# Kernel optimization log

Measured on AMD Instinct MI355X. Metric: run time of the kernel, lower is better.

The kernel has to match this reference:

```python
import jax, jax.numpy as jnp
import numpy as np

# dims / hyperparams (mirror init_kwargs)
B, N, C, K = 256, 16000, 32, 64          # batch, samples, cochlear channels, gammatone taps
FS, FMIN, FMAX, BWF = 16000, 100.0, 8000.0, 1.0
WINDOW, STRIDE = 256, 128                # inner hair cell framing -> T = 124
ANS, HID, OUT = 10, 50, 10               # auditory-nerve fanout, bushy/ic hidden, AC out
BETA, THR = 0.95, 1.0                    # snn.Leaky(beta=0.95), threshold 1.0, subtract reset
AN_LO, AN_HI, AN_THR = 0.5, 1.5, 0.5     # an_range scales + AN firing threshold

# Heaviside spike with ATan surrogate gradient (snntorch default style)
@jax.custom_vjp
def spike(u):
    return (u > 0).astype(u.dtype)

def _spike_fwd(u):
    return spike(u), u

def _spike_bwd(u, g):
    return (g / (1.0 + (jnp.pi * u) ** 2),)

spike.defvjp(_spike_fwd, _spike_bwd)

def _gammatone_bank():
    # ERB-spaced 4th-order gammatone impulse responses, unit L2 norm. [C, K]
    def hz2erb(f):
        return 21.4 * np.log10(1.0 + 0.00437 * f)
    def erb2hz(e):
        return (10.0 ** (e / 21.4) - 1.0) / 0.00437
    cfs = erb2hz(np.linspace(hz2erb(FMIN), hz2erb(FMAX), C))
    b = BWF * 1.019 * 24.7 * (4.37 * cfs / 1000.0 + 1.0)
    t = np.arange(K) / FS
    ker = (t[None, :] ** 3) * np.exp(-2 * np.pi * b[:, None] * t[None, :]) \
          * np.cos(2 * np.pi * cfs[:, None] * t[None, :])
    ker = ker / (np.linalg.norm(ker, axis=1, keepdims=True) + 1e-12)
    return jnp.asarray(ker, jnp.float32)

def setup_inputs() -> dict:
    key = jax.random.key(0)
    k1, k2, k3, k4 = jax.random.split(key, 4)
    audio = jax.random.normal(k1, (B, N), dtype=jnp.float32)
    W_bushy = jax.random.normal(k2, (HID, C * ANS), dtype=jnp.float32) / np.sqrt(C * ANS)
    W_ic = jax.random.normal(k3, (HID, HID), dtype=jnp.float32) / np.sqrt(HID)
    W_ac = jax.random.normal(k4, (OUT, HID), dtype=jnp.float32) / np.sqrt(HID)
    return {"audio": audio, "gt_kernels": _gammatone_bank(),
            "W_bushy": W_bushy, "W_ic": W_ic, "W_ac": W_ac}

def reference(audio, gt_kernels, W_bushy, W_ic, W_ac):
    # Cochlear: gammatone filterbank, [B,1,N] conv [C,1,K] SAME -> [B,C,N]
    y = jax.lax.conv_general_dilated(audio[:, None, :], gt_kernels[:, None, :],
                                     window_strides=(1,), padding="SAME")
    # InnerHairCell: half-wave rectify + moving-average framing -> [B,C,T]
    y = jnp.maximum(y, 0.0)
    env = jax.lax.reduce_window(y, 0.0, jax.lax.add,
                                (1, 1, WINDOW), (1, 1, STRIDE), "VALID") / WINDOW
    frames = jnp.transpose(env, (2, 0, 1))  # [T,B,C]
    scales = jnp.linspace(AN_LO, AN_HI, ANS, dtype=jnp.float32)

    def lif(mem, cur):
        mem = BETA * mem + cur
        spk = spike(mem - THR)
        return spk, mem - THR * spk  # subtract reset

    def step(carry, x_t):  # x_t [B,C]
        mem_b, mem_ic, mem_ac = carry
        # AuditoryNerve: ans scaled copies per channel, threshold fire -> [B, C*ANS]
        spk_an = spike(x_t[:, :, None] * scales - AN_THR).reshape(x_t.shape[0], -1)
        spk_b, mem_b = lif(mem_b, spk_an @ W_bushy.T)     # Bushy
        spk_ic, mem_ic = lif(mem_ic, spk_b @ W_ic.T)      # InferiorColliculus
        spk_ac, mem_ac = lif(mem_ac, spk_ic @ W_ac.T)     # AudioCortex
        return (mem_b, mem_ic, mem_ac), (spk_ac, mem_ac)

    bsz = audio.shape[0]
    init = (jnp.zeros((bsz, HID), audio.dtype),
            jnp.zeros((bsz, HID), audio.dtype),
            jnp.zeros((bsz, OUT), audio.dtype))
    _, (spk_rec, mem_rec) = jax.lax.scan(step, init, frames)
    # stack along dim=1 as in torch code -> [B,T,OUT]
    return jnp.transpose(spk_rec, (1, 0, 2)), jnp.transpose(mem_rec, (1, 0, 2))
```

## Files before the change

### kernel.cpp

```cpp
#include <hip/hip_runtime.h>

#define B_   256
#define N_   16000
#define C_   32
#define K_   64
#define T_   124
#define NJ   125
#define HID_ 50
#define OUT_ 10
#define TB_  1024
#define CURS 52
#define WBS  324

typedef unsigned int u32;
typedef float v2f __attribute__((ext_vector_type(2)));
struct __align__(16) f2x2 { v2f lo, hi; };

__device__ __forceinline__ float fadd(float a, float b) { return __fadd_rn(a, b); }
__device__ __forceinline__ float fmul(float a, float b) { return __fmul_rn(a, b); }
__device__ __forceinline__ float fsub(float a, float b) { return __fsub_rn(a, b); }

__device__ __forceinline__ void PKFMA(v2f& y, v2f a, const f2x2& T, int k) {
    switch (k) {
    case 0:  asm("v_pk_fma_f32 %0, %1, %2, %0 op_sel:[0,0,0] op_sel_hi:[1,0,1]"
                 : "+v"(y) : "v"(a), "s"(T.lo)); break;
    case 1:  asm("v_pk_fma_f32 %0, %1, %2, %0 op_sel:[0,1,0] op_sel_hi:[1,1,1]"
                 : "+v"(y) : "v"(a), "s"(T.lo)); break;
    case 2:  asm("v_pk_fma_f32 %0, %1, %2, %0 op_sel:[0,0,0] op_sel_hi:[1,0,1]"
                 : "+v"(y) : "v"(a), "s"(T.hi)); break;
    default: asm("v_pk_fma_f32 %0, %1, %2, %0 op_sel:[0,1,0] op_sel_hi:[1,1,1]"
                 : "+v"(y) : "v"(a), "s"(T.hi)); break;
    }
}

__global__ __launch_bounds__(256, 4) void convA(const float* __restrict__ audio,
                                                const float* __restrict__ gt,
                                                float* __restrict__ Sg) {
    __shared__ __align__(16) float abI[1280];
    __shared__ __align__(16) float ybuf[4][4][272];

    const int b = blockIdx.x, g = blockIdx.y;
    const int tid = threadIdx.x, w = tid >> 6, lane = tid & 63;
    const float* arow = audio + (size_t)b * N_;

    const int origin = (g << 10) - 32;
    for (int idx = tid; idx < 1280; idx += 256) {
        int P = idx / 640, j = idx - P * 640;
        int ii = j >> 1, h = j & 1;
        int gi = origin + (P << 9) + (h << 8) + ii;
        float v = (gi >= 0 && gi < N_) ? arow[gi] : 0.0f;
        abI[P * 640 + (j ^ (((j >> 5) & 1) << 2))] = v;
    }
    __syncthreads();

    for (int G = 0; G < 2; ++G) {
        const int rowbase = __builtin_amdgcn_readfirstlane(((w << 3) + (G << 2)) << 6);
        const float* kg = gt + rowbase;

        v2f Y[2][4][4];
#pragma unroll
        for (int P = 0; P < 2; ++P)
#pragma unroll
            for (int ch = 0; ch < 4; ++ch)
#pragma unroll
                for (int d = 0; d < 4; ++d) { Y[P][ch][d].x = 0.0f; Y[P][ch][d].y = 0.0f; }

        {
            f2x2 Tc[4];
#pragma unroll
            for (int ch = 0; ch < 4; ++ch)
                Tc[ch] = *(const f2x2*)(kg + (ch << 6));
            const int u = lane;
            const int p1 = (u << 3) ^ (((u >> 2) & 1) << 2);
#pragma unroll
            for (int P = 0; P < 2; ++P) {
                const float* abP = abI + P * 640;
                const f2x2 A0 = *(const f2x2*)(abP + p1);
                const f2x2 A1 = *(const f2x2*)(abP + (p1 ^ 4));
#pragma unroll
                for (int e = 0; e < 4; ++e) {
                    const v2f a = (e == 0) ? A0.lo : (e == 1) ? A0.hi
                                : (e == 2) ? A1.lo : A1.hi;
#pragma unroll
                    for (int ch = 0; ch < 4; ++ch)
#pragma unroll
                        for (int d = 0; d < 4; ++d) {
                            const int kb = e - 1 - d;
                            if (kb >= 0) PKFMA(Y[P][ch][d], a, Tc[ch], kb);
                        }
                }
            }
        }

#pragma unroll 1
        for (int q = 1; q < 16; ++q) {
            f2x2 Tm[4], Tc[4];
#pragma unroll
            for (int ch = 0; ch < 4; ++ch) {
                Tm[ch] = *(const f2x2*)(kg + (ch << 6) + ((q - 1) << 2));
                Tc[ch] = *(const f2x2*)(kg + (ch << 6) + (q << 2));
            }
            const int u = lane + q;
            const int p1 = (u << 3) ^ (((u >> 2) & 1) << 2);
#pragma unroll
            for (int P = 0; P < 2; ++P) {
                const float* abP = abI + P * 640;
                const f2x2 A0 = *(const f2x2*)(abP + p1);
                const f2x2 A1 = *(const f2x2*)(abP + (p1 ^ 4));
#pragma unroll
                for (int e = 0; e < 4; ++e) {
                    const v2f a = (e == 0) ? A0.lo : (e == 1) ? A0.hi
                                : (e == 2) ? A1.lo : A1.hi;
#pragma unroll
                    for (int ch = 0; ch < 4; ++ch)
#pragma unroll
                        for (int d = 0; d < 4; ++d) {
                            const int ts = e - 1 - d;
                            if (ts >= 0) PKFMA(Y[P][ch][d], a, Tc[ch], ts);
                            else         PKFMA(Y[P][ch][d], a, Tm[ch], 4 + ts);
                        }
                }
            }
        }

        {
            f2x2 Tm[4];
#pragma unroll
            for (int ch = 0; ch < 4; ++ch)
                Tm[ch] = *(const f2x2*)(kg + (ch << 6) + 60);
            const int u = lane + 16;
            const int p1 = (u << 3) ^ (((u >> 2) & 1) << 2);
#pragma unroll
            for (int P = 0; P < 2; ++P) {
                const float* abP = abI + P * 640;
                const f2x2 A0 = *(const f2x2*)(abP + p1);
                const f2x2 A1 = *(const f2x2*)(abP + (p1 ^ 4));
#pragma unroll
                for (int e = 0; e < 4; ++e) {
                    const v2f a = (e == 0) ? A0.lo : (e == 1) ? A0.hi
                                : (e == 2) ? A1.lo : A1.hi;
#pragma unroll
                    for (int ch = 0; ch < 4; ++ch)
#pragma unroll
                        for (int d = 0; d < 4; ++d) {
                            const int ts = e - 1 - d;
                            if (ts < 0) PKFMA(Y[P][ch][d], a, Tm[ch], 4 + ts);
                        }
                }
            }
        }

#pragma unroll
        for (int pp = 0; pp < 4; ++pp) {
            const int P = pp >> 1, h = pp & 1;
#pragma unroll
            for (int ch = 0; ch < 4; ++ch) {
                float4 z;
                z.x = fmaxf(h ? Y[P][ch][0].y : Y[P][ch][0].x, 0.0f);
                z.y = fmaxf(h ? Y[P][ch][1].y : Y[P][ch][1].x, 0.0f);
                z.z = fmaxf(h ? Y[P][ch][2].y : Y[P][ch][2].x, 0.0f);
                z.w = fmaxf(h ? Y[P][ch][3].y : Y[P][ch][3].x, 0.0f);
                *(float4*)(&ybuf[w][ch][((lane >> 5) * 136) + ((lane & 31) << 2)]) = z;
            }
            {
                const int ch2 = lane >> 4, blk = (lane >> 3) & 1, j = lane & 7;
                const float* yb = &ybuf[w][ch2][blk * 136 + j];
                float r = yb[0];
#pragma unroll
                for (int m = 1; m < 16; ++m) r = fadd(r, yb[m << 3]);
                float v = fadd(r, __shfl_xor(r, 1));
                v = fadd(v, __shfl_xor(v, 2));
                v = fadd(v, __shfl_xor(v, 4));
                const int jg = (g << 3) + (pp << 1) + blk;
                const int c = (w << 3) + (G << 2) + ch2;
                if (j == 0 && jg < NJ) Sg[((size_t)b * C_ + c) * NJ + jg] = v;
            }
        }
    }
}

__global__ __launch_bounds__(TB_, 1) void snnB(const float* __restrict__ Sg,
                                               const float* __restrict__ Wb,
                                               const float* __restrict__ Wic,
                                               const float* __restrict__ Wac,
                                               float* __restrict__ out) {
    __shared__ __align__(16) float sWb[HID_ * WBS];
    __shared__ __align__(16) float sWic[HID_ * 52];
    __shared__ __align__(16) float sWac[OUT_ * 52];
    __shared__ u32   mask[128 * 10];
    __shared__ __align__(16) float cur[T_ * CURS];
    __shared__ __align__(16) float icur[T_ * CURS];
    __shared__ float acur[T_ * 12];

    const int b = blockIdx.x, tid = threadIdx.x;

    for (int i4 = tid; i4 < 4000; i4 += TB_) {
        const int i = i4 << 2;
        const int r = i / 320, col = i - r * 320;
        *(float4*)(&sWb[r * WBS + col]) = *(const float4*)(Wb + i);
    }
    for (int i = tid; i < HID_ * HID_; i += TB_) {
        int r = i / 50;
        sWic[r * 52 + (i - r * 50)] = Wic[i];
    }
    for (int i = tid; i < OUT_ * HID_; i += TB_) {
        int r = i / 50;
        sWac[r * 52 + (i - r * 50)] = Wac[i];
    }

    const float* Sb = Sg + (size_t)b * C_ * NJ;
    for (int idx = tid; idx < 1280; idx += TB_) {
        if (idx >= T_ * 10) { mask[idx] = 0; continue; }
        int t = idx / 10, wd = idx - t * 10;
        u32 m = 0;
        int c_prev = -1;
        float env = 0.0f;
        for (int k = 0; k < 32; ++k) {
            int i = wd * 32 + k;
            int c = i / 10, s = i - c * 10;
            if (c != c_prev) {
                env = fmul(fadd(Sb[c * NJ + t], Sb[c * NJ + t + 1]), 0.00390625f);
                c_prev = c;
            }
            float sf = (s == 9) ? 1.5f : (float)(0.5 + (double)s * (1.0 / 9.0));
            if (fsub(fmul(env, sf), 0.5f) > 0.0f) m |= (1u << k);
        }
        mask[idx] = m;
    }
    __syncthreads();

    if (tid < 31 * 25) {
        const int t0 = tid / 25, hp = tid - t0 * 25;
        const float* wr0 = sWb + hp * WBS;
        const float* wr1 = sWb + (hp + 25) * WBS;
        const u32* mrow = mask + t0 * 10;
        v2f a0 = {0.0f, 0.0f}, a1 = {0.0f, 0.0f};
        v2f a2 = {0.0f, 0.0f}, a3 = {0.0f, 0.0f};
#pragma unroll 1
        for (int wi = 0; wi < 10; ++wi) {
            const u32 w0 = mrow[wi],       w1 = mrow[310 + wi];
            const u32 w2 = mrow[620 + wi], w3 = mrow[930 + wi];
#pragma unroll
            for (int b2 = 0; b2 < 32; ++b2) {
                const int i = (wi << 5) + b2;
                const int iw0 = __float_as_int(wr0[i]);
                const int iw1 = __float_as_int(wr1[i]);
                const int s0 = __builtin_amdgcn_sbfe((int)w0, b2, 1);
                const int s1 = __builtin_amdgcn_sbfe((int)w1, b2, 1);
                const int s2 = __builtin_amdgcn_sbfe((int)w2, b2, 1);
                const int s3 = __builtin_amdgcn_sbfe((int)w3, b2, 1);
                v2f p0, p1, p2, p3;
                p0.x = __int_as_float(iw0 & s0);  p0.y = __int_as_float(iw1 & s0);
                p1.x = __int_as_float(iw0 & s1);  p1.y = __int_as_float(iw1 & s1);
                p2.x = __int_as_float(iw0 & s2);  p2.y = __int_as_float(iw1 & s2);
                p3.x = __int_as_float(iw0 & s3);  p3.y = __int_as_float(iw1 & s3);
                a0 = a0 + p0;
                a1 = a1 + p1;
                a2 = a2 + p2;
                a3 = a3 + p3;
            }
        }
        cur[(t0     ) * CURS + hp] = a0.x;  cur[(t0     ) * CURS + hp + 25] = a0.y;
        cur[(t0 + 31) * CURS + hp] = a1.x;  cur[(t0 + 31) * CURS + hp + 25] = a1.y;
        cur[(t0 + 62) * CURS + hp] = a2.x;  cur[(t0 + 62) * CURS + hp + 25] = a2.y;
        cur[(t0 + 93) * CURS + hp] = a3.x;  cur[(t0 + 93) * CURS + hp + 25] = a3.y;
    }
    __syncthreads();

    if (tid < HID_) {
        float mem = 0.0f;
        for (int t0 = 0; t0 < 120; t0 += 8) {
            float c0[8];
#pragma unroll
            for (int k = 0; k < 8; ++k) c0[k] = cur[(t0 + k) * CURS + tid];
#pragma unroll
            for (int k = 0; k < 8; ++k) {
                float m = fadd(fmul(0.95f, mem), c0[k]);
                float sp = (fsub(m, 1.0f) > 0.0f) ? 1.0f : 0.0f;
                mem = fsub(m, sp);
                cur[(t0 + k) * CURS + tid] = sp;
            }
        }
        for (int t = 120; t < T_; ++t) {
            float m = fadd(fmul(0.95f, mem), cur[t * CURS + tid]);
            float sp = (fsub(m, 1.0f) > 0.0f) ? 1.0f : 0.0f;
            mem = fsub(m, sp);
            cur[t * CURS + tid] = sp;
        }
    }
    __syncthreads();

    if (tid < 31 * 25) {
        const int t0 = tid / 25, hp = tid - t0 * 25;
        const float* w0 = sWic + hp * 52;
        const float* w1 = sWic + (hp + 25) * 52;
        const float* sb0 = cur + (t0     ) * CURS;
        const float* sb1 = cur + (t0 + 31) * CURS;
        const float* sb2 = cur + (t0 + 62) * CURS;
        const float* sb3 = cur + (t0 + 93) * CURS;
        float A00 = 0.0f, A01 = 0.0f, A10 = 0.0f, A11 = 0.0f;
        float A20 = 0.0f, A21 = 0.0f, A30 = 0.0f, A31 = 0.0f;
#pragma unroll
        for (int g4 = 0; g4 < 12; ++g4) {
            const float4 wa = *(const float4*)(w0 + (g4 << 2));
            const float4 wb = *(const float4*)(w1 + (g4 << 2));
            const float4 s0 = *(const float4*)(sb0 + (g4 << 2));
            const float4 s1 = *(const float4*)(sb1 + (g4 << 2));
            const float4 s2 = *(const float4*)(sb2 + (g4 << 2));
            const float4 s3 = *(const float4*)(sb3 + (g4 << 2));
            A00 = fmaf(s0.x, wa.x, A00); A00 = fmaf(s0.y, wa.y, A00);
            A00 = fmaf(s0.z, wa.z, A00); A00 = fmaf(s0.w, wa.w, A00);
            A01 = fmaf(s0.x, wb.x, A01); A01 = fmaf(s0.y, wb.y, A01);
            A01 = fmaf(s0.z, wb.z, A01); A01 = fmaf(s0.w, wb.w, A01);
            A10 = fmaf(s1.x, wa.x, A10); A10 = fmaf(s1.y, wa.y, A10);
            A10 = fmaf(s1.z, wa.z, A10); A10 = fmaf(s1.w, wa.w, A10);
            A11 = fmaf(s1.x, wb.x, A11); A11 = fmaf(s1.y, wb.y, A11);
            A11 = fmaf(s1.z, wb.z, A11); A11 = fmaf(s1.w, wb.w, A11);
            A20 = fmaf(s2.x, wa.x, A20); A20 = fmaf(s2.y, wa.y, A20);
            A20 = fmaf(s2.z, wa.z, A20); A20 = fmaf(s2.w, wa.w, A20);
            A21 = fmaf(s2.x, wb.x, A21); A21 = fmaf(s2.y, wb.y, A21);
            A21 = fmaf(s2.z, wb.z, A21); A21 = fmaf(s2.w, wb.w, A21);
            A30 = fmaf(s3.x, wa.x, A30); A30 = fmaf(s3.y, wa.y, A30);
            A30 = fmaf(s3.z, wa.z, A30); A30 = fmaf(s3.w, wa.w, A30);
            A31 = fmaf(s3.x, wb.x, A31); A31 = fmaf(s3.y, wb.y, A31);
            A31 = fmaf(s3.z, wb.z, A31); A31 = fmaf(s3.w, wb.w, A31);
        }
        A00 = fmaf(sb0[48], w0[48], A00); A00 = fmaf(sb0[49], w0[49], A00);
        A01 = fmaf(sb0[48], w1[48], A01); A01 = fmaf(sb0[49], w1[49], A01);
        A10 = fmaf(sb1[48], w0[48], A10); A10 = fmaf(sb1[49], w0[49], A10);
        A11 = fmaf(sb1[48], w1[48], A11); A11 = fmaf(sb1[49], w1[49], A11);
        A20 = fmaf(sb2[48], w0[48], A20); A20 = fmaf(sb2[49], w0[49], A20);
        A21 = fmaf(sb2[48], w1[48], A21); A21 = fmaf(sb2[49], w1[49], A21);
        A30 = fmaf(sb3[48], w0[48], A30); A30 = fmaf(sb3[49], w0[49], A30);
        A31 = fmaf(sb3[48], w1[48], A31); A31 = fmaf(sb3[49], w1[49], A31);
        icur[(t0     ) * CURS + hp] = A00;  icur[(t0     ) * CURS + hp + 25] = A01;
        icur[(t0 + 31) * CURS + hp] = A10;  icur[(t0 + 31) * CURS + hp + 25] = A11;
        icur[(t0 + 62) * CURS + hp] = A20;  icur[(t0 + 62) * CURS + hp + 25] = A21;
        icur[(t0 + 93) * CURS + hp] = A30;  icur[(t0 + 93) * CURS + hp + 25] = A31;
    }
    __syncthreads();

    if (tid < HID_) {
        float mem = 0.0f;
        for (int t0 = 0; t0 < 120; t0 += 8) {
            float c0[8];
#pragma unroll
            for (int k = 0; k < 8; ++k) c0[k] = icur[(t0 + k) * CURS + tid];
#pragma unroll
            for (int k = 0; k < 8; ++k) {
                float m = fadd(fmul(0.95f, mem), c0[k]);
                float sp = (fsub(m, 1.0f) > 0.0f) ? 1.0f : 0.0f;
                mem = fsub(m, sp);
                icur[(t0 + k) * CURS + tid] = sp;
            }
        }
        for (int t = 120; t < T_; ++t) {
            float m = fadd(fmul(0.95f, mem), icur[t * CURS + tid]);
            float sp = (fsub(m, 1.0f) > 0.0f) ? 1.0f : 0.0f;
            mem = fsub(m, sp);
            icur[t * CURS + tid] = sp;
        }
    }
    __syncthreads();

    if (tid < 31 * 5) {
        const int t0 = tid / 5, op = tid - t0 * 5;
        const float* w0 = sWac + op * 52;
        const float* w1 = sWac + (op + 5) * 52;
        const float* sb0 = icur + (t0     ) * CURS;
        const float* sb1 = icur + (t0 + 31) * CURS;
        const float* sb2 = icur + (t0 + 62) * CURS;
        const float* sb3 = icur + (t0 + 93) * CURS;
        float A00 = 0.0f, A01 = 0.0f, A10 = 0.0f, A11 = 0.0f;
        float A20 = 0.0f, A21 = 0.0f, A30 = 0.0f, A31 = 0.0f;
#pragma unroll
        for (int g4 = 0; g4 < 12; ++g4) {
            const float4 wa = *(const float4*)(w0 + (g4 << 2));
            const float4 wb = *(const float4*)(w1 + (g4 << 2));
            const float4 s0 = *(const float4*)(sb0 + (g4 << 2));
            const float4 s1 = *(const float4*)(sb1 + (g4 << 2));
            const float4 s2 = *(const float4*)(sb2 + (g4 << 2));
            const float4 s3 = *(const float4*)(sb3 + (g4 << 2));
            A00 = fmaf(s0.x, wa.x, A00); A00 = fmaf(s0.y, wa.y, A00);
            A00 = fmaf(s0.z, wa.z, A00); A00 = fmaf(s0.w, wa.w, A00);
            A01 = fmaf(s0.x, wb.x, A01); A01 = fmaf(s0.y, wb.y, A01);
            A01 = fmaf(s0.z, wb.z, A01); A01 = fmaf(s0.w, wb.w, A01);
            A10 = fmaf(s1.x, wa.x, A10); A10 = fmaf(s1.y, wa.y, A10);
            A10 = fmaf(s1.z, wa.z, A10); A10 = fmaf(s1.w, wa.w, A10);
            A11 = fmaf(s1.x, wb.x, A11); A11 = fmaf(s1.y, wb.y, A11);
            A11 = fmaf(s1.z, wb.z, A11); A11 = fmaf(s1.w, wb.w, A11);
            A20 = fmaf(s2.x, wa.x, A20); A20 = fmaf(s2.y, wa.y, A20);
            A20 = fmaf(s2.z, wa.z, A20); A20 = fmaf(s2.w, wa.w, A20);
            A21 = fmaf(s2.x, wb.x, A21); A21 = fmaf(s2.y, wb.y, A21);
            A21 = fmaf(s2.z, wb.z, A21); A21 = fmaf(s2.w, wb.w, A21);
            A30 = fmaf(s3.x, wa.x, A30); A30 = fmaf(s3.y, wa.y, A30);
            A30 = fmaf(s3.z, wa.z, A30); A30 = fmaf(s3.w, wa.w, A30);
            A31 = fmaf(s3.x, wb.x, A31); A31 = fmaf(s3.y, wb.y, A31);
            A31 = fmaf(s3.z, wb.z, A31); A31 = fmaf(s3.w, wb.w, A31);
        }
        A00 = fmaf(sb0[48], w0[48], A00); A00 = fmaf(sb0[49], w0[49], A00);
        A01 = fmaf(sb0[48], w1[48], A01); A01 = fmaf(sb0[49], w1[49], A01);
        A10 = fmaf(sb1[48], w0[48], A10); A10 = fmaf(sb1[49], w0[49], A10);
        A11 = fmaf(sb1[48], w1[48], A11); A11 = fmaf(sb1[49], w1[49], A11);
        A20 = fmaf(sb2[48], w0[48], A20); A20 = fmaf(sb2[49], w0[49], A20);
        A21 = fmaf(sb2[48], w1[48], A21); A21 = fmaf(sb2[49], w1[49], A21);
        A30 = fmaf(sb3[48], w0[48], A30); A30 = fmaf(sb3[49], w0[49], A30);
        A31 = fmaf(sb3[48], w1[48], A31); A31 = fmaf(sb3[49], w1[49], A31);
        acur[(t0     ) * 12 + op] = A00;  acur[(t0     ) * 12 + op + 5] = A01;
        acur[(t0 + 31) * 12 + op] = A10;  acur[(t0 + 31) * 12 + op + 5] = A11;
        acur[(t0 + 62) * 12 + op] = A20;  acur[(t0 + 62) * 12 + op + 5] = A21;
        acur[(t0 + 93) * 12 + op] = A30;  acur[(t0 + 93) * 12 + op + 5] = A31;
    }
    __syncthreads();

    if (tid < OUT_) {
        float mem = 0.0f;
        for (int t0 = 0; t0 < 120; t0 += 8) {
            float c0[8];
#pragma unroll
            for (int k = 0; k < 8; ++k) c0[k] = acur[(t0 + k) * 12 + tid];
#pragma unroll
            for (int k = 0; k < 8; ++k) {
                float m = fadd(fmul(0.95f, mem), c0[k]);
                float sp = (fsub(m, 1.0f) > 0.0f) ? 1.0f : 0.0f;
                float mo = fsub(m, sp);
                mem = mo;
                size_t base = ((size_t)b * T_ + (t0 + k)) * OUT_ + tid;
                out[base] = sp;
                out[(size_t)(B_ * T_ * OUT_) + base] = mo;
            }
        }
        for (int t = 120; t < T_; ++t) {
            float m = fadd(fmul(0.95f, mem), acur[t * 12 + tid]);
            float sp = (fsub(m, 1.0f) > 0.0f) ? 1.0f : 0.0f;
            float mo = fsub(m, sp);
            mem = mo;
            size_t base = ((size_t)b * T_ + t) * OUT_ + tid;
            out[base] = sp;
            out[(size_t)(B_ * T_ * OUT_) + base] = mo;
        }
    }
}

extern "C" void kernel_launch(void* const* d_in, const int* in_sizes, int n_in,
                              void* d_out, int out_size, void* d_ws, size_t ws_size,
                              hipStream_t stream) {
    (void)in_sizes; (void)n_in; (void)out_size; (void)ws_size;
    const float* audio = (const float*)d_in[0];
    const float* gt    = (const float*)d_in[1];
    const float* Wb    = (const float*)d_in[2];
    const float* Wic   = (const float*)d_in[3];
    const float* Wac   = (const float*)d_in[4];

    float* Sg = (float*)d_ws;

    convA<<<dim3(B_, 16), dim3(256), 0, stream>>>(audio, gt, Sg);
    snnB<<<dim3(B_), dim3(TB_), 0, stream>>>(Sg, Wb, Wic, Wac, (float*)d_out);
}
```

Before: 290.7 us.

## Split SNN kernel into time-parallel bushy-current kernel and recurrent kernel

The single per-batch SNN kernel is split in two. The first kernel computes the bushy-layer input currents with two blocks per batch item, each covering half of the timesteps, and writes them to workspace memory. The second kernel loads those currents and runs the recurrent LIF layers. This spreads the dominant masked matmul over twice as many blocks to use more CUs, at the cost of an extra launch and a global round-trip for the currents. The original fused kernel is kept as a fallback when the workspace is too small.

Result: no change. 285.9 us (-1.7%).

```diff
diff --git a/kernel.cpp b/kernel.cpp
--- a/kernel.cpp
+++ b/kernel.cpp
@@ -11,6 +11,7 @@
 #define TB_  1024
 #define CURS 52
 #define WBS  324
+#define TSPAN 62
 
 typedef unsigned int u32;
 typedef float v2f __attribute__((ext_vector_type(2)));
@@ -179,39 +180,27 @@
     }
 }
 
-__global__ __launch_bounds__(TB_, 1) void snnB(const float* __restrict__ Sg,
-                                               const float* __restrict__ Wb,
-                                               const float* __restrict__ Wic,
-                                               const float* __restrict__ Wac,
-                                               float* __restrict__ out) {
+__global__ __launch_bounds__(1024, 8) void snnB1(const float* __restrict__ Sg,
+                                                 const float* __restrict__ Wb,
+                                                 float* __restrict__ cur2) {
     __shared__ __align__(16) float sWb[HID_ * WBS];
-    __shared__ __align__(16) float sWic[HID_ * 52];
-    __shared__ __align__(16) float sWac[OUT_ * 52];
-    __shared__ u32   mask[128 * 10];
-    __shared__ __align__(16) float cur[T_ * CURS];
-    __shared__ __align__(16) float icur[T_ * CURS];
-    __shared__ float acur[T_ * 12];
-
-    const int b = blockIdx.x, tid = threadIdx.x;
-
-    for (int i4 = tid; i4 < 4000; i4 += TB_) {
+    __shared__ u32 mask[64 * 10];
+
+    const int b = blockIdx.x, tg = blockIdx.y;
+    const int tid = threadIdx.x;
+    const int tbase = tg * TSPAN;
+
+    for (int i4 = tid; i4 < 4000; i4 += 1024) {
         const int i = i4 << 2;
         const int r = i / 320, col = i - r * 320;
         *(float4*)(&sWb[r * WBS + col]) = *(const float4*)(Wb + i);
     }
-    for (int i = tid; i < HID_ * HID_; i += TB_) {
-        int r = i / 50;
-        sWic[r * 52 + (i - r * 50)] = Wic[i];
-    }
-    for (int i = tid; i < OUT_ * HID_; i += TB_) {
-        int r = i / 50;
-        sWac[r * 52 + (i - r * 50)] = Wac[i];
-    }
 
     const float* Sb = Sg + (size_t)b * C_ * NJ;
-    for (int idx = tid; idx < 1280; idx += TB_) {
-        if (idx >= T_ * 10) { mask[idx] = 0; continue; }
-        int t = idx / 10, wd = idx - t * 10;
+    for (int idx = tid; idx < 640; idx += 1024) {
+        if (idx >= TSPAN * 10) { mask[idx] = 0; continue; }
+        int tl = idx / 10, wd = idx - tl * 10;
+        int t = tbase + tl;
         u32 m = 0;
         int c_prev = -1;
         float env = 0.0f;
@@ -230,40 +219,59 @@
     __syncthreads();
 
     if (tid < 31 * 25) {
-        const int t0 = tid / 25, hp = tid - t0 * 25;
+        const int tl = tid / 25, hp = tid - tl * 25;
         const float* wr0 = sWb + hp * WBS;
         const float* wr1 = sWb + (hp + 25) * WBS;
-        const u32* mrow = mask + t0 * 10;
-        v2f a0 = {0.0f, 0.0f}, a1 = {0.0f, 0.0f};
-        v2f a2 = {0.0f, 0.0f}, a3 = {0.0f, 0.0f};
+        const u32* mA = mask + tl * 10;
+        const u32* mB = mask + (tl + 31) * 10;
+        v2f A0 = {0.0f, 0.0f}, A1 = {0.0f, 0.0f};
 #pragma unroll 1
         for (int wi = 0; wi < 10; ++wi) {
-            const u32 w0 = mrow[wi],       w1 = mrow[310 + wi];
-            const u32 w2 = mrow[620 + wi], w3 = mrow[930 + wi];
+            const u32 wa = mA[wi], wc = mB[wi];
 #pragma unroll
             for (int b2 = 0; b2 < 32; ++b2) {
                 const int i = (wi << 5) + b2;
                 const int iw0 = __float_as_int(wr0[i]);
                 const int iw1 = __float_as_int(wr1[i]);
-                const int s0 = __builtin_amdgcn_sbfe((int)w0, b2, 1);
-                const int s1 = __builtin_amdgcn_sbfe((int)w1, b2, 1);
-                const int s2 = __builtin_amdgcn_sbfe((int)w2, b2, 1);
-                const int s3 = __builtin_amdgcn_sbfe((int)w3, b2, 1);
-                v2f p0, p1, p2, p3;
-                p0.x = __int_as_float(iw0 & s0);  p0.y = __int_as_float(iw1 & s0);
-                p1.x = __int_as_float(iw0 & s1);  p1.y = __int_as_float(iw1 & s1);
-                p2.x = __int_as_float(iw0 & s2);  p2.y = __int_as_float(iw1 & s2);
-                p3.x = __int_as_float(iw0 & s3);  p3.y = __int_as_float(iw1 & s3);
-                a0 = a0 + p0;
-                a1 = a1 + p1;
-                a2 = a2 + p2;
-                a3 = a3 + p3;
-            }
-        }
-        cur[(t0     ) * CURS + hp] = a0.x;  cur[(t0     ) * CURS + hp + 25] = a0.y;
-        cur[(t0 + 31) * CURS + hp] = a1.x;  cur[(t0 + 31) * CURS + hp + 25] = a1.y;
-        cur[(t0 + 62) * CURS + hp] = a2.x;  cur[(t0 + 62) * CURS + hp + 25] = a2.y;
-        cur[(t0 + 93) * CURS + hp] = a3.x;  cur[(t0 + 93) * CURS + hp + 25] = a3.y;
+                const int sa = __builtin_amdgcn_sbfe((int)wa, b2, 1);
+                const int sc = __builtin_amdgcn_sbfe((int)wc, b2, 1);
+                v2f p0, p1;
+                p0.x = __int_as_float(iw0 & sa);  p0.y = __int_as_float(iw1 & sa);
+                p1.x = __int_as_float(iw0 & sc);  p1.y = __int_as_float(iw1 & sc);
+                A0 = A0 + p0;
+                A1 = A1 + p1;
+            }
+        }
+        float* cb = cur2 + ((size_t)b * T_ + tbase) * HID_;
+        cb[(tl     ) * HID_ + hp] = A0.x;  cb[(tl     ) * HID_ + hp + 25] = A0.y;
+        cb[(tl + 31) * HID_ + hp] = A1.x;  cb[(tl + 31) * HID_ + hp + 25] = A1.y;
+    }
+}
+
+__global__ __launch_bounds__(1024, 1) void snnB2(const float* __restrict__ cur2,
+                                                 const float* __restrict__ Wic,
+                                                 const float* __restrict__ Wac,
+                                                 float* __restrict__ out) {
+    __shared__ __align__(16) float sWic[HID_ * 52];
+    __shared__ __align__(16) float sWac[OUT_ * 52];
+    __shared__ __align__(16) float cur[T_ * CURS];
+    __shared__ __align__(16) float icur[T_ * CURS];
+    __shared__ float acur[T_ * 12];
+
+    const int b = blockIdx.x, tid = threadIdx.x;
+
+    for (int i = tid; i < HID_ * HID_; i += 1024) {
+        int r = i / 50;
+        sWic[r * 52 + (i - r * 50)] = Wic[i];
+    }
+    for (int i = tid; i < OUT_ * HID_; i += 1024) {
+        int r = i / 50;
+        sWac[r * 52 + (i - r * 50)] = Wac[i];
+    }
+    const float* cb = cur2 + (size_t)b * T_ * HID_;
+    for (int j = tid; j < T_ * 25; j += 1024) {
+        int t = j / 25, h2 = (j - t * 25) << 1;
+        *(float2*)(&cur[t * CURS + h2]) = *(const float2*)(cb + t * HID_ + h2);
     }
     __syncthreads();
 
@@ -442,10 +450,273 @@
     }
 }
 
+__global__ __launch_bounds__(TB_, 1) void snnB(const float* __restrict__ Sg,
+                                               const float* __restrict__ Wb,
+                                               const float* __restrict__ Wic,
+                                               const float* __restrict__ Wac,
+                                               float* __restrict__ out) {
+    __shared__ __align__(16) float sWb[HID_ * WBS];
+    __shared__ __align__(16) float sWic[HID_ * 52];
+    __shared__ __align__(16) float sWac[OUT_ * 52];
+    __shared__ u32   mask[128 * 10];
+    __shared__ __align__(16) float cur[T_ * CURS];
+    __shared__ __align__(16) float icur[T_ * CURS];
+    __shared__ float acur[T_ * 12];
+
+    const int b = blockIdx.x, tid = threadIdx.x;
+
+    for (int i4 = tid; i4 < 4000; i4 += TB_) {
+        const int i = i4 << 2;
+        const int r = i / 320, col = i - r * 320;
+        *(float4*)(&sWb[r * WBS + col]) = *(const float4*)(Wb + i);
+    }
+    for (int i = tid; i < HID_ * HID_; i += TB_) {
+        int r = i / 50;
+        sWic[r * 52 + (i - r * 50)] = Wic[i];
+    }
+    for (int i = tid; i < OUT_ * HID_; i += TB_) {
+        int r = i / 50;
+        sWac[r * 52 + (i - r * 50)] = Wac[i];
+    }
+
+    const float* Sb = Sg + (size_t)b * C_ * NJ;
+    for (int idx = tid; idx < 1280; idx += TB_) {
+        if (idx >= T_ * 10) { mask[idx] = 0; continue; }
+        int t = idx / 10, wd = idx - t * 10;
+        u32 m = 0;
+        int c_prev = -1;
+        float env = 0.0f;
+        for (int k = 0; k < 32; ++k) {
+            int i = wd * 32 + k;
+            int c = i / 10, s = i - c * 10;
+            if (c != c_prev) {
+                env = fmul(fadd(Sb[c * NJ + t], Sb[c * NJ + t + 1]), 0.00390625f);
+                c_prev = c;
+            }
+            float sf = (s == 9) ? 1.5f : (float)(0.5 + (double)s * (1.0 / 9.0));
+            if (fsub(fmul(env, sf), 0.5f) > 0.0f) m |= (1u << k);
+        }
+        mask[idx] = m;
+    }
+    __syncthreads();
+
+    if (tid < 31 * 25) {
+        const int t0 = tid / 25, hp = tid - t0 * 25;
+        const float* wr0 = sWb + hp * WBS;
+        const float* wr1 = sWb + (hp + 25) * WBS;
+        const u32* mrow = mask + t0 * 10;
+        v2f a0 = {0.0f, 0.0f}, a1 = {0.0f, 0.0f};
+        v2f a2 = {0.0f, 0.0f}, a3 = {0.0f, 0.0f};
+#pragma unroll 1
+        for (int wi = 0; wi < 10; ++wi) {
+            const u32 w0 = mrow[wi],       w1 = mrow[310 + wi];
+            const u32 w2 = mrow[620 + wi], w3 = mrow[930 + wi];
+#pragma unroll
+            for (int b2 = 0; b2 < 32; ++b2) {
+                const int i = (wi << 5) + b2;
+                const int iw0 = __float_as_int(wr0[i]);
+                const int iw1 = __float_as_int(wr1[i]);
+                const int s0 = __builtin_amdgcn_sbfe((int)w0, b2, 1);
+                const int s1 = __builtin_amdgcn_sbfe((int)w1, b2, 1);
+                const int s2 = __builtin_amdgcn_sbfe((int)w2, b2, 1);
+                const int s3 = __builtin_amdgcn_sbfe((int)w3, b2, 1);
+                v2f p0, p1, p2, p3;
+                p0.x = __int_as_float(iw0 & s0);  p0.y = __int_as_float(iw1 & s0);
+                p1.x = __int_as_float(iw0 & s1);  p1.y = __int_as_float(iw1 & s1);
+                p2.x = __int_as_float(iw0 & s2);  p2.y = __int_as_float(iw1 & s2);
+                p3.x = __int_as_float(iw0 & s3);  p3.y = __int_as_float(iw1 & s3);
+                a0 = a0 + p0;
+                a1 = a1 + p1;
+                a2 = a2 + p2;
+                a3 = a3 + p3;
+            }
+        }
+        cur[(t0     ) * CURS + hp] = a0.x;  cur[(t0     ) * CURS + hp + 25] = a0.y;
+        cur[(t0 + 31) * CURS + hp] = a1.x;  cur[(t0 + 31) * CURS + hp + 25] = a1.y;
+        cur[(t0 + 62) * CURS + hp] = a2.x;  cur[(t0 + 62) * CURS + hp + 25] = a2.y;
+        cur[(t0 + 93) * CURS + hp] = a3.x;  cur[(t0 + 93) * CURS + hp + 25] = a3.y;
+    }
+    __syncthreads();
+
+    if (tid < HID_) {
+        float mem = 0.0f;
+        for (int t0 = 0; t0 < 120; t0 += 8) {
+            float c0[8];
+#pragma unroll
+            for (int k = 0; k < 8; ++k) c0[k] = cur[(t0 + k) * CURS + tid];
+#pragma unroll
+            for (int k = 0; k < 8; ++k) {
+                float m = fadd(fmul(0.95f, mem), c0[k]);
+                float sp = (fsub(m, 1.0f) > 0.0f) ? 1.0f : 0.0f;
+                mem = fsub(m, sp);
+                cur[(t0 + k) * CURS + tid] = sp;
+            }
+        }
+        for (int t = 120; t < T_; ++t) {
+            float m = fadd(fmul(0.95f, mem), cur[t * CURS + tid]);
+            float sp = (fsub(m, 1.0f) > 0.0f) ? 1.0f : 0.0f;
+            mem = fsub(m, sp);
+            cur[t * CURS + tid] = sp;
+        }
+    }
+    __syncthreads();
+
+    if (tid < 31 * 25) {
+        const int t0 = tid / 25, hp = tid - t0 * 25;
+        const float* w0 = sWic + hp * 52;
+        const float* w1 = sWic + (hp + 25) * 52;
+        const float* sb0 = cur + (t0     ) * CURS;
+        const float* sb1 = cur + (t0 + 31) * CURS;
+        const float* sb2 = cur + (t0 + 62) * CURS;
+        const float* sb3 = cur + (t0 + 93) * CURS;
+        float A00 = 0.0f, A01 = 0.0f, A10 = 0.0f, A11 = 0.0f;
+        float A20 = 0.0f, A21 = 0.0f, A30 = 0.0f, A31 = 0.0f;
+#pragma unroll
+        for (int g4 = 0; g4 < 12; ++g4) {
+            const float4 wa = *(const float4*)(w0 + (g4 << 2));
+            const float4 wb = *(const float4*)(w1 + (g4 << 2));
+            const float4 s0 = *(const float4*)(sb0 + (g4 << 2));
+            const float4 s1 = *(const float4*)(sb1 + (g4 << 2));
+            const float4 s2 = *(const float4*)(sb2 + (g4 << 2));
+            const float4 s3 = *(const float4*)(sb3 + (g4 << 2));
+            A00 = fmaf(s0.x, wa.x, A00); A00 = fmaf(s0.y, wa.y, A00);
+            A00 = fmaf(s0.z, wa.z, A00); A00 = fmaf(s0.w, wa.w, A00);
+            A01 = fmaf(s0.x, wb.x, A01); A01 = fmaf(s0.y, wb.y, A01);
+            A01 = fmaf(s0.z, wb.z, A01); A01 = fmaf(s0.w, wb.w, A01);
+            A10 = fmaf(s1.x, wa.x, A10); A10 = fmaf(s1.y, wa.y, A10);
+            A10 = fmaf(s1.z, wa.z, A10); A10 = fmaf(s1.w, wa.w, A10);
+            A11 = fmaf(s1.x, wb.x, A11); A11 = fmaf(s1.y, wb.y, A11);
+            A11 = fmaf(s1.z, wb.z, A11); A11 = fmaf(s1.w, wb.w, A11);
+            A20 = fmaf(s2.x, wa.x, A20); A20 = fmaf(s2.y, wa.y, A20);
+            A20 = fmaf(s2.z, wa.z, A20); A20 = fmaf(s2.w, wa.w, A20);
+            A21 = fmaf(s2.x, wb.x, A21); A21 = fmaf(s2.y, wb.y, A21);
+            A21 = fmaf(s2.z, wb.z, A21); A21 = fmaf(s2.w, wb.w, A21);
+            A30 = fmaf(s3.x, wa.x, A30); A30 = fmaf(s3.y, wa.y, A30);
+            A30 = fmaf(s3.z, wa.z, A30); A30 = fmaf(s3.w, wa.w, A30);
+            A31 = fmaf(s3.x, wb.x, A31); A31 = fmaf(s3.y, wb.y, A31);
+            A31 = fmaf(s3.z, wb.z, A31); A31 = fmaf(s3.w, wb.w, A31);
+        }
+        A00 = fmaf(sb0[48], w0[48], A00); A00 = fmaf(sb0[49], w0[49], A00);
+        A01 = fmaf(sb0[48], w1[48], A01); A01 = fmaf(sb0[49], w1[49], A01);
+        A10 = fmaf(sb1[48], w0[48], A10); A10 = fmaf(sb1[49], w0[49], A10);
+        A11 = fmaf(sb1[48], w1[48], A11); A11 = fmaf(sb1[49], w1[49], A11);
+        A20 = fmaf(sb2[48], w0[48], A20); A20 = fmaf(sb2[49], w0[49], A20);
+        A21 = fmaf(sb2[48], w1[48], A21); A21 = fmaf(sb2[49], w1[49], A21);
+        A30 = fmaf(sb3[48], w0[48], A30); A30 = fmaf(sb3[49], w0[49], A30);
+        A31 = fmaf(sb3[48], w1[48], A31); A31 = fmaf(sb3[49], w1[49], A31);
+        icur[(t0     ) * CURS + hp] = A00;  icur[(t0     ) * CURS + hp + 25] = A01;
+        icur[(t0 + 31) * CURS + hp] = A10;  icur[(t0 + 31) * CURS + hp + 25] = A11;
+        icur[(t0 + 62) * CURS + hp] = A20;  icur[(t0 + 62) * CURS + hp + 25] = A21;
+        icur[(t0 + 93) * CURS + hp] = A30;  icur[(t0 + 93) * CURS + hp + 25] = A31;
+    }
+    __syncthreads();
+
+    if (tid < HID_) {
+        float mem = 0.0f;
+        for (int t0 = 0; t0 < 120; t0 += 8) {
+            float c0[8];
+#pragma unroll
+            for (int k = 0; k < 8; ++k) c0[k] = icur[(t0 + k) * CURS + tid];
+#pragma unroll
+            for (int k = 0; k < 8; ++k) {
+                float m = fadd(fmul(0.95f, mem), c0[k]);
+                float sp = (fsub(m, 1.0f) > 0.0f) ? 1.0f : 0.0f;
+                mem = fsub(m, sp);
+                icur[(t0 + k) * CURS + tid] = sp;
+            }
+        }
+        for (int t = 120; t < T_; ++t) {
+            float m = fadd(fmul(0.95f, mem), icur[t * CURS + tid]);
+            float sp = (fsub(m, 1.0f) > 0.0f) ? 1.0f : 0.0f;
+            mem = fsub(m, sp);
+            icur[t * CURS + tid] = sp;
+        }
+    }
+    __syncthreads();
+
+    if (tid < 31 * 5) {
+        const int t0 = tid / 5, op = tid - t0 * 5;
+        const float* w0 = sWac + op * 52;
+        const float* w1 = sWac + (op + 5) * 52;
+        const float* sb0 = icur + (t0     ) * CURS;
+        const float* sb1 = icur + (t0 + 31) * CURS;
+        const float* sb2 = icur + (t0 + 62) * CURS;
+        const float* sb3 = icur + (t0 + 93) * CURS;
+        float A00 = 0.0f, A01 = 0.0f, A10 = 0.0f, A11 = 0.0f;
+        float A20 = 0.0f, A21 = 0.0f, A30 = 0.0f, A31 = 0.0f;
+#pragma unroll
+        for (int g4 = 0; g4 < 12; ++g4) {
+            const float4 wa = *(const float4*)(w0 + (g4 << 2));
+            const float4 wb = *(const float4*)(w1 + (g4 << 2));
+            const float4 s0 = *(const float4*)(sb0 + (g4 << 2));
+            const float4 s1 = *(const float4*)(sb1 + (g4 << 2));
+            const float4 s2 = *(const float4*)(sb2 + (g4 << 2));
+            const float4 s3 = *(const float4*)(sb3 + (g4 << 2));
+            A00 = fmaf(s0.x, wa.x, A00); A00 = fmaf(s0.y, wa.y, A00);
+            A00 = fmaf(s0.z, wa.z, A00); A00 = fmaf(s0.w, wa.w, A00);
+            A01 = fmaf(s0.x, wb.x, A01); A01 = fmaf(s0.y, wb.y, A01);
+            A01 = fmaf(s0.z, wb.z, A01); A01 = fmaf(s0.w, wb.w, A01);
+            A10 = fmaf(s1.x, wa.x, A10); A10 = fmaf(s1.y, wa.y, A10);
+            A10 = fmaf(s1.z, wa.z, A10); A10 = fmaf(s1.w, wa.w, A10);
+            A11 = fmaf(s1.x, wb.x, A11); A11 = fmaf(s1.y, wb.y, A11);
+            A11 = fmaf(s1.z, wb.z, A11); A11 = fmaf(s1.w, wb.w, A11);
+            A20 = fmaf(s2.x, wa.x, A20); A20 = fmaf(s2.y, wa.y, A20);
+            A20 = fmaf(s2.z, wa.z, A20); A20 = fmaf(s2.w, wa.w, A20);
+            A21 = fmaf(s2.x, wb.x, A21); A21 = fmaf(s2.y, wb.y, A21);
+            A21 = fmaf(s2.z, wb.z, A21); A21 = fmaf(s2.w, wb.w, A21);
+            A30 = fmaf(s3.x, wa.x, A30); A30 = fmaf(s3.y, wa.y, A30);
+            A30 = fmaf(s3.z, wa.z, A30); A30 = fmaf(s3.w, wa.w, A30);
+            A31 = fmaf(s3.x, wb.x, A31); A31 = fmaf(s3.y, wb.y, A31);
+            A31 = fmaf(s3.z, wb.z, A31); A31 = fmaf(s3.w, wb.w, A31);
+        }
+        A00 = fmaf(sb0[48], w0[48], A00); A00 = fmaf(sb0[49], w0[49], A00);
+        A01 = fmaf(sb0[48], w1[48], A01); A01 = fmaf(sb0[49], w1[49], A01);
+        A10 = fmaf(sb1[48], w0[48], A10); A10 = fmaf(sb1[49], w0[49], A10);
+        A11 = fmaf(sb1[48], w1[48], A11); A11 = fmaf(sb1[49], w1[49], A11);
+        A20 = fmaf(sb2[48], w0[48], A20); A20 = fmaf(sb2[49], w0[49], A20);
+        A21 = fmaf(sb2[48], w1[48], A21); A21 = fmaf(sb2[49], w1[49], A21);
+        A30 = fmaf(sb3[48], w0[48], A30); A30 = fmaf(sb3[49], w0[49], A30);
+        A31 = fmaf(sb3[48], w1[48], A31); A31 = fmaf(sb3[49], w1[49], A31);
+        acur[(t0     ) * 12 + op] = A00;  acur[(t0     ) * 12 + op + 5] = A01;
+        acur[(t0 + 31) * 12 + op] = A10;  acur[(t0 + 31) * 12 + op + 5] = A11;
+        acur[(t0 + 62) * 12 + op] = A20;  acur[(t0 + 62) * 12 + op + 5] = A21;
+        acur[(t0 + 93) * 12 + op] = A30;  acur[(t0 + 93) * 12 + op + 5] = A31;
+    }
+    __syncthreads();
+
+    if (tid < OUT_) {
+        float mem = 0.0f;
+        for (int t0 = 0; t0 < 120; t0 += 8) {
+            float c0[8];
+#pragma unroll
+            for (int k = 0; k < 8; ++k) c0[k] = acur[(t0 + k) * 12 + tid];
+#pragma unroll
+            for (int k = 0; k < 8; ++k) {
+                float m = fadd(fmul(0.95f, mem), c0[k]);
+                float sp = (fsub(m, 1.0f) > 0.0f) ? 1.0f : 0.0f;
+                float mo = fsub(m, sp);
+                mem = mo;
+                size_t base = ((size_t)b * T_ + (t0 + k)) * OUT_ + tid;
+                out[base] = sp;
+                out[(size_t)(B_ * T_ * OUT_) + base] = mo;
+            }
+        }
+        for (int t = 120; t < T_; ++t) {
+            float m = fadd(fmul(0.95f, mem), acur[t * 12 + tid]);
+            float sp = (fsub(m, 1.0f) > 0.0f) ? 1.0f : 0.0f;
+            float mo = fsub(m, sp);
+            mem = mo;
+            size_t base = ((size_t)b * T_ + t) * OUT_ + tid;
+            out[base] = sp;
+            out[(size_t)(B_ * T_ * OUT_) + base] = mo;
+        }
+    }
+}
+
 extern "C" void kernel_launch(void* const* d_in, const int* in_sizes, int n_in,
                               void* d_out, int out_size, void* d_ws, size_t ws_size,
                               hipStream_t stream) {
-    (void)in_sizes; (void)n_in; (void)out_size; (void)ws_size;
+    (void)in_sizes; (void)n_in; (void)out_size;
     const float* audio = (const float*)d_in[0];
     const float* gt    = (const float*)d_in[1];
     const float* Wb    = (const float*)d_in[2];
@@ -453,7 +724,16 @@
     const float* Wac   = (const float*)d_in[4];
 
     float* Sg = (float*)d_ws;
+    const size_t SG_BYTES  = (size_t)B_ * C_ * NJ * 4;
+    const size_t CUR_BYTES = (size_t)B_ * T_ * HID_ * 4;
 
     convA<<<dim3(B_, 16), dim3(256), 0, stream>>>(audio, gt, Sg);
-    snnB<<<dim3(B_), dim3(TB_), 0, stream>>>(Sg, Wb, Wic, Wac, (float*)d_out);
+
+    if (ws_size >= SG_BYTES + CUR_BYTES) {
+        float* cur2 = (float*)((char*)d_ws + SG_BYTES);
+        snnB1<<<dim3(B_, 2), dim3(1024), 0, stream>>>(Sg, Wb, cur2);
+        snnB2<<<dim3(B_), dim3(1024), 0, stream>>>(cur2, Wic, Wac, (float*)d_out);
+    } else {
+        snnB<<<dim3(B_), dim3(TB_), 0, stream>>>(Sg, Wb, Wic, Wac, (float*)d_out);
+    }
 }
```

## Pad shared strides to odd values and precompute per-channel spike patterns in snnB

Applied to the files above, without the earlier changes.

Changes the shared-memory row strides to odd values (53, 321) so that strided accesses across threads avoid LDS bank conflicts. Drops the float4 vector loads in favour of scalar loops and remaps threads so that consecutive lanes walk the time axis. The AN spike masks now come from a precomputed 10-bit pattern per channel and timestep, stored temporarily in the cur buffer, instead of re-evaluating the envelope for every bit. Mask words are also preloaded into registers before the bushy accumulation loop. In exchange the code gives up 128-bit LDS loads and adds an extra barrier.

New measurement: 290.8 us. Within noise of the previous version (+0.0%).

```diff
diff --git a/kernel.cpp b/kernel.cpp
--- a/kernel.cpp
+++ b/kernel.cpp
@@ -9,8 +9,8 @@
 #define HID_ 50
 #define OUT_ 10
 #define TB_  1024
-#define CURS 52
-#define WBS  324
+#define CURS 53
+#define WBS  321
 
 typedef unsigned int u32;
 typedef float v2f __attribute__((ext_vector_type(2)));
@@ -184,46 +184,58 @@
                                                const float* __restrict__ Wic,
                                                const float* __restrict__ Wac,
                                                float* __restrict__ out) {
-    __shared__ __align__(16) float sWb[HID_ * WBS];
-    __shared__ __align__(16) float sWic[HID_ * 52];
-    __shared__ __align__(16) float sWac[OUT_ * 52];
-    __shared__ u32   mask[128 * 10];
+    __shared__ float sWb[HID_ * WBS];
+    __shared__ float sWic[HID_ * CURS];
+    __shared__ float sWac[OUT_ * CURS];
+    __shared__ u32   mask[1280];
     __shared__ __align__(16) float cur[T_ * CURS];
     __shared__ __align__(16) float icur[T_ * CURS];
     __shared__ float acur[T_ * 12];
 
     const int b = blockIdx.x, tid = threadIdx.x;
-
-    for (int i4 = tid; i4 < 4000; i4 += TB_) {
-        const int i = i4 << 2;
-        const int r = i / 320, col = i - r * 320;
-        *(float4*)(&sWb[r * WBS + col]) = *(const float4*)(Wb + i);
+    u32* patt = (u32*)cur;
+
+    for (int i = tid; i < HID_ * 320; i += TB_) {
+        int r = i / 320;
+        sWb[r * WBS + (i - r * 320)] = Wb[i];
     }
     for (int i = tid; i < HID_ * HID_; i += TB_) {
         int r = i / 50;
-        sWic[r * 52 + (i - r * 50)] = Wic[i];
+        sWic[r * CURS + (i - r * 50)] = Wic[i];
     }
     for (int i = tid; i < OUT_ * HID_; i += TB_) {
         int r = i / 50;
-        sWac[r * 52 + (i - r * 50)] = Wac[i];
+        sWac[r * CURS + (i - r * 50)] = Wac[i];
     }
 
     const float* Sb = Sg + (size_t)b * C_ * NJ;
+    for (int idx = tid; idx < C_ * T_; idx += TB_) {
+        int c = idx / T_, t = idx - c * T_;
+        float env = fmul(fadd(Sb[c * NJ + t], Sb[c * NJ + t + 1]), 0.00390625f);
+        u32 p = 0;
+#pragma unroll
+        for (int s = 0; s < 10; ++s) {
+            const float sf = (s == 9) ? 1.5f : (float)(0.5 + (double)s * (1.0 / 9.0));
+            if (fsub(fmul(env, sf), 0.5f) > 0.0f) p |= (1u << s);
+        }
+        patt[c * 128 + t] = p;
+    }
+    __syncthreads();
+
     for (int idx = tid; idx < 1280; idx += TB_) {
         if (idx >= T_ * 10) { mask[idx] = 0; continue; }
         int t = idx / 10, wd = idx - t * 10;
+        const int bit0 = wd << 5;
+        const int c0 = bit0 / 10;
         u32 m = 0;
-        int c_prev = -1;
-        float env = 0.0f;
-        for (int k = 0; k < 32; ++k) {
-            int i = wd * 32 + k;
-            int c = i / 10, s = i - c * 10;
-            if (c != c_prev) {
-                env = fmul(fadd(Sb[c * NJ + t], Sb[c * NJ + t + 1]), 0.00390625f);
-                c_prev = c;
-            }
-            float sf = (s == 9) ? 1.5f : (float)(0.5 + (double)s * (1.0 / 9.0));
-            if (fsub(fmul(env, sf), 0.5f) > 0.0f) m |= (1u << k);
+#pragma unroll
+        for (int cc = 0; cc < 5; ++cc) {
+            int c = c0 + cc;
+            int sh = c * 10 - bit0;
+            if (c < C_ && sh < 32) {
+                u32 p = patt[c * 128 + t];
+                m |= (sh >= 0) ? (p << sh) : (p >> (-sh));
+            }
         }
         mask[idx] = m;
     }
@@ -236,10 +248,18 @@
         const u32* mrow = mask + t0 * 10;
         v2f a0 = {0.0f, 0.0f}, a1 = {0.0f, 0.0f};
         v2f a2 = {0.0f, 0.0f}, a3 = {0.0f, 0.0f};
+        u32 wbuf0[10], wbuf1[10], wbuf2[10], wbuf3[10];
+#pragma unroll
+        for (int wi = 0; wi < 10; ++wi) {
+            wbuf0[wi] = mrow[wi];
+            wbuf1[wi] = mrow[310 + wi];
+            wbuf2[wi] = mrow[620 + wi];
+            wbuf3[wi] = mrow[930 + wi];
+        }
 #pragma unroll 1
         for (int wi = 0; wi < 10; ++wi) {
-            const u32 w0 = mrow[wi],       w1 = mrow[310 + wi];
-            const u32 w2 = mrow[620 + wi], w3 = mrow[930 + wi];
+            const u32 w0 = wbuf0[wi], w1 = wbuf1[wi];
+            const u32 w2 = wbuf2[wi], w3 = wbuf3[wi];
 #pragma unroll
             for (int b2 = 0; b2 < 32; ++b2) {
                 const int i = (wi << 5) + b2;
@@ -291,52 +311,28 @@
     __syncthreads();
 
     if (tid < 31 * 25) {
-        const int t0 = tid / 25, hp = tid - t0 * 25;
-        const float* w0 = sWic + hp * 52;
-        const float* w1 = sWic + (hp + 25) * 52;
-        const float* sb0 = cur + (t0     ) * CURS;
-        const float* sb1 = cur + (t0 + 31) * CURS;
-        const float* sb2 = cur + (t0 + 62) * CURS;
-        const float* sb3 = cur + (t0 + 93) * CURS;
+        const int hp = tid / 31, tl = tid - hp * 31;
+        const float* w0 = sWic + hp * CURS;
+        const float* w1 = sWic + (hp + 25) * CURS;
+        const float* sb0 = cur + (tl     ) * CURS;
+        const float* sb1 = cur + (tl + 31) * CURS;
+        const float* sb2 = cur + (tl + 62) * CURS;
+        const float* sb3 = cur + (tl + 93) * CURS;
         float A00 = 0.0f, A01 = 0.0f, A10 = 0.0f, A11 = 0.0f;
         float A20 = 0.0f, A21 = 0.0f, A30 = 0.0f, A31 = 0.0f;
-#pragma unroll
-        for (int g4 = 0; g4 < 12; ++g4) {
-            const float4 wa = *(const float4*)(w0 + (g4 << 2));
-            const float4 wb = *(const float4*)(w1 + (g4 << 2));
-            const float4 s0 = *(const float4*)(sb0 + (g4 << 2));
-            const float4 s1 = *(const float4*)(sb1 + (g4 << 2));
-            const float4 s2 = *(const float4*)(sb2 + (g4 << 2));
-            const float4 s3 = *(const float4*)(sb3 + (g4 << 2));
-            A00 = fmaf(s0.x, wa.x, A00); A00 = fmaf(s0.y, wa.y, A00);
-            A00 = fmaf(s0.z, wa.z, A00); A00 = fmaf(s0.w, wa.w, A00);
-            A01 = fmaf(s0.x, wb.x, A01); A01 = fmaf(s0.y, wb.y, A01);
-            A01 = fmaf(s0.z, wb.z, A01); A01 = fmaf(s0.w, wb.w, A01);
-            A10 = fmaf(s1.x, wa.x, A10); A10 = fmaf(s1.y, wa.y, A10);
-            A10 = fmaf(s1.z, wa.z, A10); A10 = fmaf(s1.w, wa.w, A10);
-            A11 = fmaf(s1.x, wb.x, A11); A11 = fmaf(s1.y, wb.y, A11);
-            A11 = fmaf(s1.z, wb.z, A11); A11 = fmaf(s1.w, wb.w, A11);
-            A20 = fmaf(s2.x, wa.x, A20); A20 = fmaf(s2.y, wa.y, A20);
-            A20 = fmaf(s2.z, wa.z, A20); A20 = fmaf(s2.w, wa.w, A20);
-            A21 = fmaf(s2.x, wb.x, A21); A21 = fmaf(s2.y, wb.y, A21);
-            A21 = fmaf(s2.z, wb.z, A21); A21 = fmaf(s2.w, wb.w, A21);
-            A30 = fmaf(s3.x, wa.x, A30); A30 = fmaf(s3.y, wa.y, A30);
-            A30 = fmaf(s3.z, wa.z, A30); A30 = fmaf(s3.w, wa.w, A30);
-            A31 = fmaf(s3.x, wb.x, A31); A31 = fmaf(s3.y, wb.y, A31);
-            A31 = fmaf(s3.z, wb.z, A31); A31 = fmaf(s3.w, wb.w, A31);
-        }
-        A00 = fmaf(sb0[48], w0[48], A00); A00 = fmaf(sb0[49], w0[49], A00);
-        A01 = fmaf(sb0[48], w1[48], A01); A01 = fmaf(sb0[49], w1[49], A01);
-        A10 = fmaf(sb1[48], w0[48], A10); A10 = fmaf(sb1[49], w0[49], A10);
-        A11 = fmaf(sb1[48], w1[48], A11); A11 = fmaf(sb1[49], w1[49], A11);
-        A20 = fmaf(sb2[48], w0[48], A20); A20 = fmaf(sb2[49], w0[49], A20);
-        A21 = fmaf(sb2[48], w1[48], A21); A21 = fmaf(sb2[49], w1[49], A21);
-        A30 = fmaf(sb3[48], w0[48], A30); A30 = fmaf(sb3[49], w0[49], A30);
-        A31 = fmaf(sb3[48], w1[48], A31); A31 = fmaf(sb3[49], w1[49], A31);
-        icur[(t0     ) * CURS + hp] = A00;  icur[(t0     ) * CURS + hp + 25] = A01;
-        icur[(t0 + 31) * CURS + hp] = A10;  icur[(t0 + 31) * CURS + hp + 25] = A11;
-        icur[(t0 + 62) * CURS + hp] = A20;  icur[(t0 + 62) * CURS + hp + 25] = A21;
-        icur[(t0 + 93) * CURS + hp] = A30;  icur[(t0 + 93) * CURS + hp + 25] = A31;
+#pragma unroll 10
+        for (int g = 0; g < HID_; ++g) {
+            const float wa = w0[g], wb = w1[g];
+            const float s0 = sb0[g], s1 = sb1[g], s2 = sb2[g], s3 = sb3[g];
+            A00 = fmaf(s0, wa, A00);  A01 = fmaf(s0, wb, A01);
+            A10 = fmaf(s1, wa, A10);  A11 = fmaf(s1, wb, A11);
+            A20 = fmaf(s2, wa, A20);  A21 = fmaf(s2, wb, A21);
+            A30 = fmaf(s3, wa, A30);  A31 = fmaf(s3, wb, A31);
+        }
+        icur[(tl     ) * CURS + hp] = A00;  icur[(tl     ) * CURS + hp + 25] = A01;
+        icur[(tl + 31) * CURS + hp] = A10;  icur[(tl + 31) * CURS + hp + 25] = A11;
+        icur[(tl + 62) * CURS + hp] = A20;  icur[(tl + 62) * CURS + hp + 25] = A21;
+        icur[(tl + 93) * CURS + hp] = A30;  icur[(tl + 93) * CURS + hp + 25] = A31;
     }
     __syncthreads();
 
@@ -364,52 +360,28 @@
     __syncthreads();
 
     if (tid < 31 * 5) {
-        const int t0 = tid / 5, op = tid - t0 * 5;
-        const float* w0 = sWac + op * 52;
-        const float* w1 = sWac + (op + 5) * 52;
-        const float* sb0 = icur + (t0     ) * CURS;
-        const float* sb1 = icur + (t0 + 31) * CURS;
-        const float* sb2 = icur + (t0 + 62) * CURS;
-        const float* sb3 = icur + (t0 + 93) * CURS;
+        const int op = tid / 31, tl = tid - op * 31;
+        const float* w0 = sWac + op * CURS;
+        const float* w1 = sWac + (op + 5) * CURS;
+        const float* sb0 = icur + (tl     ) * CURS;
+        const float* sb1 = icur + (tl + 31) * CURS;
+        const float* sb2 = icur + (tl + 62) * CURS;
+        const float* sb3 = icur + (tl + 93) * CURS;
         float A00 = 0.0f, A01 = 0.0f, A10 = 0.0f, A11 = 0.0f;
         float A20 = 0.0f, A21 = 0.0f, A30 = 0.0f, A31 = 0.0f;
-#pragma unroll
-        for (int g4 = 0; g4 < 12; ++g4) {
-            const float4 wa = *(const float4*)(w0 + (g4 << 2));
-            const float4 wb = *(const float4*)(w1 + (g4 << 2));
-            const float4 s0 = *(const float4*)(sb0 + (g4 << 2));
-            const float4 s1 = *(const float4*)(sb1 + (g4 << 2));
-            const float4 s2 = *(const float4*)(sb2 + (g4 << 2));
-            const float4 s3 = *(const float4*)(sb3 + (g4 << 2));
-            A00 = fmaf(s0.x, wa.x, A00); A00 = fmaf(s0.y, wa.y, A00);
-            A00 = fmaf(s0.z, wa.z, A00); A00 = fmaf(s0.w, wa.w, A00);
-            A01 = fmaf(s0.x, wb.x, A01); A01 = fmaf(s0.y, wb.y, A01);
-            A01 = fmaf(s0.z, wb.z, A01); A01 = fmaf(s0.w, wb.w, A01);
-            A10 = fmaf(s1.x, wa.x, A10); A10 = fmaf(s1.y, wa.y, A10);
-            A10 = fmaf(s1.z, wa.z, A10); A10 = fmaf(s1.w, wa.w, A10);
-            A11 = fmaf(s1.x, wb.x, A11); A11 = fmaf(s1.y, wb.y, A11);
-            A11 = fmaf(s1.z, wb.z, A11); A11 = fmaf(s1.w, wb.w, A11);
-            A20 = fmaf(s2.x, wa.x, A20); A20 = fmaf(s2.y, wa.y, A20);
-            A20 = fmaf(s2.z, wa.z, A20); A20 = fmaf(s2.w, wa.w, A20);
-            A21 = fmaf(s2.x, wb.x, A21); A21 = fmaf(s2.y, wb.y, A21);
-            A21 = fmaf(s2.z, wb.z, A21); A21 = fmaf(s2.w, wb.w, A21);
-            A30 = fmaf(s3.x, wa.x, A30); A30 = fmaf(s3.y, wa.y, A30);
-            A30 = fmaf(s3.z, wa.z, A30); A30 = fmaf(s3.w, wa.w, A30);
-            A31 = fmaf(s3.x, wb.x, A31); A31 = fmaf(s3.y, wb.y, A31);
-            A31 = fmaf(s3.z, wb.z, A31); A31 = fmaf(s3.w, wb.w, A31);
-        }
-        A00 = fmaf(sb0[48], w0[48], A00); A00 = fmaf(sb0[49], w0[49], A00);
-        A01 = fmaf(sb0[48], w1[48], A01); A01 = fmaf(sb0[49], w1[49], A01);
-        A10 = fmaf(sb1[48], w0[48], A10); A10 = fmaf(sb1[49], w0[49], A10);
-        A11 = fmaf(sb1[48], w1[48], A11); A11 = fmaf(sb1[49], w1[49], A11);
-        A20 = fmaf(sb2[48], w0[48], A20); A20 = fmaf(sb2[49], w0[49], A20);
-        A21 = fmaf(sb2[48], w1[48], A21); A21 = fmaf(sb2[49], w1[49], A21);
-        A30 = fmaf(sb3[48], w0[48], A30); A30 = fmaf(sb3[49], w0[49], A30);
-        A31 = fmaf(sb3[48], w1[48], A31); A31 = fmaf(sb3[49], w1[49], A31);
-        acur[(t0     ) * 12 + op] = A00;  acur[(t0     ) * 12 + op + 5] = A01;
-        acur[(t0 + 31) * 12 + op] = A10;  acur[(t0 + 31) * 12 + op + 5] = A11;
-        acur[(t0 + 62) * 12 + op] = A20;  acur[(t0 + 62) * 12 + op + 5] = A21;
-        acur[(t0 + 93) * 12 + op] = A30;  acur[(t0 + 93) * 12 + op + 5] = A31;
+#pragma unroll 10
+        for (int g = 0; g < HID_; ++g) {
+            const float wa = w0[g], wb = w1[g];
+            const float s0 = sb0[g], s1 = sb1[g], s2 = sb2[g], s3 = sb3[g];
+            A00 = fmaf(s0, wa, A00);  A01 = fmaf(s0, wb, A01);
+            A10 = fmaf(s1, wa, A10);  A11 = fmaf(s1, wb, A11);
+            A20 = fmaf(s2, wa, A20);  A21 = fmaf(s2, wb, A21);
+            A30 = fmaf(s3, wa, A30);  A31 = fmaf(s3, wb, A31);
+        }
+        acur[(tl     ) * 12 + op] = A00;  acur[(tl     ) * 12 + op + 5] = A01;
+        acur[(tl + 31) * 12 + op] = A10;  acur[(tl + 31) * 12 + op + 5] = A11;
+        acur[(tl + 62) * 12 + op] = A20;  acur[(tl + 62) * 12 + op + 5] = A21;
+        acur[(tl + 93) * 12 + op] = A30;  acur[(tl + 93) * 12 + op + 5] = A31;
     }
     __syncthreads();
 
```
